# Kernel optimization log

Hardware: AMD Instinct MI355X
Metric: run time of the kernel (lower is better)

The kernel has to match this reference:

```python
import jax, jax.numpy as jnp
import numpy as np

B, T, D = 8, 4096, 768
N_HEADS = 12
HEAD_DIM = D // N_HEADS
N_STATE = 64
ALPHA = 0.1


def setup_inputs() -> dict:
    key = jax.random.key(0)
    k1, k2, k3 = jax.random.split(key, 3)
    H = jax.random.normal(k1, (B, T, D), dtype=jnp.float32)
    prototypes = jax.random.normal(k2, (N_STATE, D), dtype=jnp.float32)
    W_tok = jax.random.normal(k3, (D, D), dtype=jnp.float32) * (1.0 / np.sqrt(D))
    s0 = jnp.zeros((1, N_STATE, D), dtype=jnp.float32)
    return {"H": H, "prototypes": prototypes, "W_tok": W_tok, "s0": s0}


def reference(H, prototypes, W_tok, s0):
    b, t, d = H.shape
    hd = HEAD_DIM
    a = ALPHA
    # q: [B, n_heads, T, head_dim]
    q = (H @ W_tok.T).reshape(b, t, N_HEADS, hd).transpose(0, 2, 1, 3)
    # k: [n_heads, n_state, head_dim]
    k = prototypes.reshape(N_STATE, N_HEADS, hd).transpose(1, 0, 2)
    # score: [B, n_heads, T, n_state]; routing_temp == 1.0
    score = jnp.einsum('bhtd,hmd->bhtm', q, k) / (hd ** 0.5)
    w = jax.nn.softmax(score, axis=-1)
    g = 1.0 - a * w
    # suffix-inclusive product over T: prod_{t'>=t} g[t']
    suffix_inc = jnp.flip(jnp.cumprod(jnp.flip(g, axis=2), axis=2), axis=2)
    suffix_exc = jnp.concatenate(
        [suffix_inc[:, :, 1:, :], jnp.ones_like(suffix_inc[:, :, :1, :])], axis=2)
    w_eff = a * w * suffix_exc  # [B, H, T, n_state]
    h_ph = H.reshape(b, t, N_HEADS, hd).transpose(0, 2, 1, 3)  # [B,H,T,hd]
    s0h = jnp.broadcast_to(s0, (b, N_STATE, d)).reshape(
        b, N_STATE, N_HEADS, hd).transpose(0, 2, 1, 3)  # [B,H,n_state,hd]
    residual = suffix_inc[:, :, 0, :][..., None]  # [B,H,n_state,1]
    s = s0h * residual + jnp.einsum('bhtm,bhtd->bhmd', w_eff, h_ph)
    return s.transpose(0, 2, 1, 3).reshape(b, N_STATE, d)
```

## Files before the change

kernel.cpp:

```cpp
#include <hip/hip_runtime.h>

#define B_ 8
#define T_ 4096
#define D_ 768
#define NH_ 12
#define M_ 64
#define ALPHA_ 0.1f

#define CCH 16
#define CHUNK_T 256

using half8 = __attribute__((ext_vector_type(8))) _Float16;
using short8 = __attribute__((ext_vector_type(8))) short;
using f32x4 = __attribute__((ext_vector_type(4))) float;

__device__ __forceinline__ unsigned int f2h2(float a, float b) {
    unsigned short ua = __builtin_bit_cast(unsigned short, (_Float16)a);
    unsigned short ub = __builtin_bit_cast(unsigned short, (_Float16)b);
    return (unsigned int)ua | ((unsigned int)ub << 16);
}
__device__ __forceinline__ float h2f(unsigned short u) {
    return (float)__builtin_bit_cast(_Float16, u);
}
__device__ __forceinline__ void gload_lds16(const void* g, void* l) {
    __builtin_amdgcn_global_load_lds(
        (const __attribute__((address_space(1))) unsigned int*)g,
        (__attribute__((address_space(3))) unsigned int*)l, 16, 0, 0);
}

__global__ __launch_bounds__(256) void kH16(const float* __restrict__ H,
                                            unsigned short* __restrict__ H16) {
    const int i = blockIdx.x * 256 + threadIdx.x;
#pragma unroll
    for (int j = 0; j < 4; ++j) {
        const int idx = i + j * 1572864;
        const float4 v = reinterpret_cast<const float4*>(H)[idx];
        uint2 pk = {f2h2(v.x, v.y), f2h2(v.z, v.w)};
        reinterpret_cast<uint2*>(H16)[idx] = pk;
    }
}

__global__ __launch_bounds__(256) void kP(const float* __restrict__ proto,
                                          const float* __restrict__ W,
                                          unsigned short* __restrict__ P16) {
    const int et = blockIdx.x;
    const int h  = blockIdx.y;
    const int tid = threadIdx.x;

    __shared__ __align__(16) float Ws[64 * 128];
    __shared__ __align__(16) float Ks[64 * 64];

#pragma unroll
    for (int j = 0; j < 8; ++j) {
        int f = tid + j * 256;
        int i = f >> 5, c4 = f & 31;
        const float4 v = *reinterpret_cast<const float4*>(
            W + (size_t)(h * 64 + i) * D_ + et * 128 + c4 * 4);
        *reinterpret_cast<float4*>(&Ws[i * 128 + c4 * 4]) = v;
    }
#pragma unroll
    for (int j = 0; j < 4; ++j) {
        int f = tid + j * 256;
        int m = f >> 4, i4 = f & 15;
        const float4 v = *reinterpret_cast<const float4*>(
            proto + (size_t)m * D_ + h * 64 + i4 * 4);
        Ks[(i4 * 4 + 0) * 64 + m] = v.x;
        Ks[(i4 * 4 + 1) * 64 + m] = v.y;
        Ks[(i4 * 4 + 2) * 64 + m] = v.z;
        Ks[(i4 * 4 + 3) * 64 + m] = v.w;
    }
    __syncthreads();

    const int m0 = (tid >> 5) * 8;
    const int e0 = (tid & 31) * 4;
    float acc[8][4];
#pragma unroll
    for (int i = 0; i < 8; ++i)
#pragma unroll
        for (int j = 0; j < 4; ++j) acc[i][j] = 0.f;

    for (int i = 0; i < 64; ++i) {
        const float4 bb = *reinterpret_cast<const float4*>(&Ws[i * 128 + e0]);
        const float4 a0 = *reinterpret_cast<const float4*>(&Ks[i * 64 + m0]);
        const float4 a1 = *reinterpret_cast<const float4*>(&Ks[i * 64 + m0 + 4]);
        const float a[8] = {a0.x, a0.y, a0.z, a0.w, a1.x, a1.y, a1.z, a1.w};
#pragma unroll
        for (int mi = 0; mi < 8; ++mi) {
            acc[mi][0] = fmaf(a[mi], bb.x, acc[mi][0]);
            acc[mi][1] = fmaf(a[mi], bb.y, acc[mi][1]);
            acc[mi][2] = fmaf(a[mi], bb.z, acc[mi][2]);
            acc[mi][3] = fmaf(a[mi], bb.w, acc[mi][3]);
        }
    }
#pragma unroll
    for (int mi = 0; mi < 8; ++mi) {
        size_t idx = (size_t)(h * 64 + m0 + mi) * D_ + et * 128 + e0;
        uint2 pk = {f2h2(acc[mi][0] * 0.125f, acc[mi][1] * 0.125f),
                    f2h2(acc[mi][2] * 0.125f, acc[mi][3] * 0.125f)};
        *reinterpret_cast<uint2*>(P16 + idx) = pk;
    }
}

#define LDS_BYTES 69632

__global__ __launch_bounds__(512, 4) void k1(const unsigned short* __restrict__ H16,
                                             const unsigned short* __restrict__ P16,
                                             float* __restrict__ chunkprod,
                                             float* __restrict__ partial) {
    const int p = blockIdx.x;
    const int b = p & 7;
    const int s = p >> 3;
    const int hp = s % 6;
    const int c  = s / 6;
    const int tid = threadIdx.x;
    const int wv  = tid >> 6;
    const int lane = tid & 63;
    const int l15 = lane & 15;
    const int q4  = lane >> 4;
    const int hl  = wv >> 2;
    const int tq  = wv & 3;

    extern __shared__ __align__(16) unsigned char smem[];
    unsigned short* wT = (unsigned short*)(smem);
    unsigned short* Hh = (unsigned short*)(smem + 33792);
    float* segprod = (float*)(smem + 67584);

    const size_t Hrow = (size_t)(b * T_ + c * CHUNK_T);
    const unsigned short* gA = H16 + Hrow * D_;
    const unsigned short* gB = P16 + (size_t)(hp * 2) * 64 * D_;

    f32x4 acc[4][4] = {};

    for (int kt = 0; kt < 12; ++kt) {
        __syncthreads();
#pragma unroll
        for (int j = 0; j < 4; ++j) {
            int sl = j * 512 + tid;
            int r = sl >> 3, gp = sl & 7, g = gp ^ (r & 7);
            gload_lds16(gA + (size_t)r * D_ + kt * 64 + g * 8, smem + sl * 16);
        }
#pragma unroll
        for (int j = 0; j < 2; ++j) {
            int sl = j * 512 + tid;
            int r = (sl & 511) >> 3, gp = sl & 7, g = gp ^ (r & 7);
            gload_lds16(gB + (size_t)(j * 64 + r) * D_ + kt * 64 + g * 8,
                        smem + 32768 + sl * 16);
        }
        __syncthreads();
#pragma unroll
        for (int ks = 0; ks < 2; ++ks) {
            const int gp = ((ks * 4 + q4) ^ (l15 & 7)) * 16;
            half8 af[4], bf[4];
#pragma unroll
            for (int tt = 0; tt < 4; ++tt)
                af[tt] = *reinterpret_cast<const half8*>(
                    smem + (tq * 64 + tt * 16 + l15) * 128 + gp);
#pragma unroll
            for (int mt = 0; mt < 4; ++mt)
                bf[mt] = *reinterpret_cast<const half8*>(
                    smem + 32768 + hl * 8192 + (mt * 16 + l15) * 128 + gp);
#pragma unroll
            for (int tt = 0; tt < 4; ++tt)
#pragma unroll
                for (int mt = 0; mt < 4; ++mt)
                    acc[tt][mt] = __builtin_amdgcn_mfma_f32_16x16x32_f16(
                        af[tt], bf[mt], acc[tt][mt], 0, 0, 0);
        }
    }

#pragma unroll
    for (int tt = 0; tt < 4; ++tt)
#pragma unroll
        for (int rg = 0; rg < 4; ++rg) {
            float e0 = __expf(acc[tt][0][rg]);
            float e1 = __expf(acc[tt][1][rg]);
            float e2 = __expf(acc[tt][2][rg]);
            float e3 = __expf(acc[tt][3][rg]);
            float sm = (e0 + e1) + (e2 + e3);
#pragma unroll
            for (int msk = 1; msk <= 8; msk <<= 1)
                sm += __shfl_xor(sm, msk, 64);
            float inv = __builtin_amdgcn_rcpf(sm);
            acc[tt][0][rg] = e0 * inv;
            acc[tt][1][rg] = e1 * inv;
            acc[tt][2][rg] = e2 * inv;
            acc[tt][3][rg] = e3 * inv;
        }
    __syncthreads();

    const int m_s = tid & 63;
    const int g8  = tid >> 6;

    for (int head = 0; head < 2; ++head) {
        const int h = hp * 2 + head;
        const int chunkIdx = (b * NH_ + h) * CCH + c;
        if (head) __syncthreads();

        if (hl == head) {
#pragma unroll
            for (int tt = 0; tt < 4; ++tt)
#pragma unroll
                for (int mt = 0; mt < 4; ++mt) {
                    uint2 pk = {f2h2(acc[tt][mt][0], acc[tt][mt][1]),
                                f2h2(acc[tt][mt][2], acc[tt][mt][3])};
                    *reinterpret_cast<uint2*>(
                        wT + (mt * 16 + l15) * 264 + tq * 64 + tt * 16 + q4 * 4) = pk;
                }
        }
        {
            const int dp = tid & 31, tg = tid >> 5;
            const unsigned short* src = H16 + (Hrow + tg * 16) * D_ + h * 64 + 2 * dp;
            unsigned short* dst0 = Hh + (2 * dp) * 264 + tg * 16;
            unsigned short* dst1 = Hh + (2 * dp + 1) * 264 + tg * 16;
#pragma unroll
            for (int i = 0; i < 8; ++i) {
                unsigned int a = *reinterpret_cast<const unsigned int*>(
                    src + (size_t)(2 * i) * D_);
                unsigned int bb = *reinterpret_cast<const unsigned int*>(
                    src + (size_t)(2 * i + 1) * D_);
                *reinterpret_cast<unsigned int*>(dst0 + 2 * i) =
                    (a & 0xffffu) | (bb << 16);
                *reinterpret_cast<unsigned int*>(dst1 + 2 * i) =
                    (a >> 16) | (bb & 0xffff0000u);
            }
        }
        __syncthreads();

        {
            unsigned short* rowp = wT + m_s * 264 + g8 * 32;
            float pband = 1.0f;
#pragma unroll
            for (int oct = 0; oct < 4; ++oct) {
                short8 v = *reinterpret_cast<const short8*>(rowp + oct * 8);
#pragma unroll
                for (int j = 0; j < 8; ++j)
                    pband *= fmaf(-ALPHA_, h2f((unsigned short)v[j]), 1.0f);
            }
            segprod[g8 * 64 + m_s] = pband;
            __syncthreads();
            float R = 1.0f;
#pragma unroll
            for (int gg = 1; gg < 8; ++gg)
                if (g8 + gg < 8) R *= segprod[(g8 + gg) * 64 + m_s];
            if (g8 == 0)
                chunkprod[(size_t)chunkIdx * 64 + m_s] = R * pband;
#pragma unroll
            for (int oct = 3; oct >= 0; --oct) {
                short8 v = *reinterpret_cast<const short8*>(rowp + oct * 8);
                short8 o;
#pragma unroll
                for (int j = 7; j >= 0; --j) {
                    float w = h2f((unsigned short)v[j]);
                    _Float16 we = (_Float16)(ALPHA_ * w * R);
                    o[j] = (short)__builtin_bit_cast(unsigned short, we);
                    R *= fmaf(-ALPHA_, w, 1.0f);
                }
                *reinterpret_cast<short8*>(rowp + oct * 8) = o;
            }
        }
        __syncthreads();

        {
            const int mt = wv & 3;
            const int dh = wv >> 2;
            f32x4 pacc[2] = {};
#pragma unroll
            for (int ks = 0; ks < 8; ++ks) {
                half8 a = *reinterpret_cast<const half8*>(
                    wT + (mt * 16 + l15) * 264 + ks * 32 + q4 * 8);
#pragma unroll
                for (int dt = 0; dt < 2; ++dt) {
                    half8 bb = *reinterpret_cast<const half8*>(
                        Hh + (dh * 32 + dt * 16 + l15) * 264 + ks * 32 + q4 * 8);
                    pacc[dt] = __builtin_amdgcn_mfma_f32_16x16x32_f16(
                        a, bb, pacc[dt], 0, 0, 0);
                }
            }
#pragma unroll
            for (int dt = 0; dt < 2; ++dt)
#pragma unroll
                for (int rg = 0; rg < 4; ++rg)
                    partial[((size_t)chunkIdx * 64 + mt * 16 + q4 * 4 + rg) * 64
                            + dh * 32 + dt * 16 + l15] = pacc[dt][rg];
        }
    }
}

__global__ __launch_bounds__(256) void k2(const float* __restrict__ chunkprod,
                                          const float* __restrict__ partial,
                                          const float* __restrict__ s0,
                                          float* __restrict__ out) {
    const int h = blockIdx.x;
    const int b = blockIdx.y;
    const int mg = blockIdx.z;
    const int tid = threadIdx.x;
    const int m  = mg * 16 + (tid >> 4);
    const int d0 = (tid & 15) * 4;

    const size_t cpBase = (size_t)(b * NH_ + h) * CCH;
    float sfx[CCH];
    float run = 1.0f;
#pragma unroll
    for (int c = CCH - 1; c >= 0; --c) {
        sfx[c] = run;
        run *= chunkprod[(cpBase + c) * M_ + m];
    }
    const float4 v0 = *reinterpret_cast<const float4*>(
        s0 + (size_t)m * D_ + h * 64 + d0);
    float4 acc = make_float4(v0.x * run, v0.y * run, v0.z * run, v0.w * run);
#pragma unroll
    for (int c = 0; c < CCH; ++c) {
        const float sv = sfx[c];
        const float4 pp = *reinterpret_cast<const float4*>(
            partial + ((cpBase + c) * M_ + m) * 64 + d0);
        acc.x = fmaf(sv, pp.x, acc.x);
        acc.y = fmaf(sv, pp.y, acc.y);
        acc.z = fmaf(sv, pp.z, acc.z);
        acc.w = fmaf(sv, pp.w, acc.w);
    }
    *reinterpret_cast<float4*>(out + (size_t)(b * M_ + m) * D_ + h * 64 + d0) = acc;
}

extern "C" void kernel_launch(void* const* d_in, const int* in_sizes, int n_in,
                              void* d_out, int out_size, void* d_ws, size_t ws_size,
                              hipStream_t stream) {
    const float* H     = (const float*)d_in[0];
    const float* proto = (const float*)d_in[1];
    const float* W     = (const float*)d_in[2];
    const float* s0    = (const float*)d_in[3];
    float* out = (float*)d_out;

    unsigned short* H16 = (unsigned short*)d_ws;
    unsigned short* P16 = (unsigned short*)((unsigned char*)d_ws + 50331648);
    float* chunkprod = (float*)((unsigned char*)d_ws + 51511296);
    float* partial   = (float*)((unsigned char*)d_ws + 51904512);

    kH16<<<dim3(6144), 256, 0, stream>>>(H, H16);
    kP<<<dim3(6, NH_), 256, 0, stream>>>(proto, W, P16);
    k1<<<dim3(768), 512, LDS_BYTES, stream>>>(H16, P16, chunkprod, partial);
    k2<<<dim3(NH_, B_, 4), 256, 0, stream>>>(chunkprod, partial, s0, out);
}
```

Measured before the change: 226.7 us.

## Double-buffer k1 score GEMM with 32x32 MFMA and prefetch head slices

The score GEMM in k1 now stages 32-wide K slices into two alternating LDS buffers, so global-to-LDS copies for the next step overlap MFMA work on the current one, with one barrier per iteration instead of two. It also switches from 16x16x32 to 32x32x16 f16 MFMA tiles and adapts the softmax reduction and the transposed write-out to the new accumulator layout. The H slices for both heads are loaded into registers early, overlapping them with the softmax and head-0 work. Most block barriers are replaced by an LDS-only wait plus s_barrier, so pending global loads are not drained at each barrier. This raises register pressure, and the ordering of the loads relies on the new barriers being correct.

```diff
diff --git a/kernel.cpp b/kernel.cpp
--- a/kernel.cpp
+++ b/kernel.cpp
@@ -13,6 +13,7 @@
 using half8 = __attribute__((ext_vector_type(8))) _Float16;
 using short8 = __attribute__((ext_vector_type(8))) short;
 using f32x4 = __attribute__((ext_vector_type(4))) float;
+using f32x16 = __attribute__((ext_vector_type(16))) float;
 
 __device__ __forceinline__ unsigned int f2h2(float a, float b) {
     unsigned short ua = __builtin_bit_cast(unsigned short, (_Float16)a);
@@ -26,6 +27,10 @@
     __builtin_amdgcn_global_load_lds(
         (const __attribute__((address_space(1))) unsigned int*)g,
         (__attribute__((address_space(3))) unsigned int*)l, 16, 0, 0);
+}
+__device__ __forceinline__ void barrier_lgkm() {
+    asm volatile("s_waitcnt lgkmcnt(0)" ::: "memory");
+    __builtin_amdgcn_s_barrier();
 }
 
 __global__ __launch_bounds__(256) void kH16(const float* __restrict__ H,
@@ -102,6 +107,22 @@
 }
 
 #define LDS_BYTES 69632
+
+#define STAGE(KT, BUF) do {                                                    \
+    _Pragma("unroll")                                                          \
+    for (int j_ = 0; j_ < 2; ++j_) {                                           \
+        int sl_ = j_ * 512 + tid;                                              \
+        int r_ = sl_ >> 2, gp_ = sl_ & 3, g_ = gp_ ^ ((r_ >> 1) & 3);          \
+        gload_lds16(gA + (size_t)r_ * D_ + (KT) * 32 + g_ * 8,                 \
+                    smem + (BUF) * 16384 + sl_ * 16);                          \
+    }                                                                          \
+    {                                                                          \
+        int sl_ = tid;                                                         \
+        int r_ = sl_ >> 2, gp_ = sl_ & 3, g_ = gp_ ^ ((r_ >> 1) & 3);          \
+        gload_lds16(gB + (size_t)r_ * D_ + (KT) * 32 + g_ * 8,                 \
+                    smem + 32768 + (BUF) * 8192 + sl_ * 16);                   \
+    }                                                                          \
+} while (0)
 
 __global__ __launch_bounds__(512, 4) void k1(const unsigned short* __restrict__ H16,
                                              const unsigned short* __restrict__ P16,
@@ -117,6 +138,8 @@
     const int lane = tid & 63;
     const int l15 = lane & 15;
     const int q4  = lane >> 4;
+    const int l31 = lane & 31;
+    const int q1  = lane >> 5;
     const int hl  = wv >> 2;
     const int tq  = wv & 3;
 
@@ -129,64 +152,63 @@
     const unsigned short* gA = H16 + Hrow * D_;
     const unsigned short* gB = P16 + (size_t)(hp * 2) * 64 * D_;
 
-    f32x4 acc[4][4] = {};
-
-    for (int kt = 0; kt < 12; ++kt) {
+    f32x16 acc2[2][2] = {};
+
+    const int sx = (l31 >> 1) & 3;
+    STAGE(0, 0);
+    for (int kt = 0; kt < 24; ++kt) {
         __syncthreads();
-#pragma unroll
-        for (int j = 0; j < 4; ++j) {
-            int sl = j * 512 + tid;
-            int r = sl >> 3, gp = sl & 7, g = gp ^ (r & 7);
-            gload_lds16(gA + (size_t)r * D_ + kt * 64 + g * 8, smem + sl * 16);
-        }
-#pragma unroll
-        for (int j = 0; j < 2; ++j) {
-            int sl = j * 512 + tid;
-            int r = (sl & 511) >> 3, gp = sl & 7, g = gp ^ (r & 7);
-            gload_lds16(gB + (size_t)(j * 64 + r) * D_ + kt * 64 + g * 8,
-                        smem + 32768 + sl * 16);
-        }
-        __syncthreads();
-#pragma unroll
-        for (int ks = 0; ks < 2; ++ks) {
-            const int gp = ((ks * 4 + q4) ^ (l15 & 7)) * 16;
-            half8 af[4], bf[4];
-#pragma unroll
-            for (int tt = 0; tt < 4; ++tt)
-                af[tt] = *reinterpret_cast<const half8*>(
-                    smem + (tq * 64 + tt * 16 + l15) * 128 + gp);
-#pragma unroll
-            for (int mt = 0; mt < 4; ++mt)
-                bf[mt] = *reinterpret_cast<const half8*>(
-                    smem + 32768 + hl * 8192 + (mt * 16 + l15) * 128 + gp);
-#pragma unroll
-            for (int tt = 0; tt < 4; ++tt)
-#pragma unroll
-                for (int mt = 0; mt < 4; ++mt)
-                    acc[tt][mt] = __builtin_amdgcn_mfma_f32_16x16x32_f16(
-                        af[tt], bf[mt], acc[tt][mt], 0, 0, 0);
-        }
-    }
-
-#pragma unroll
-    for (int tt = 0; tt < 4; ++tt)
-#pragma unroll
-        for (int rg = 0; rg < 4; ++rg) {
-            float e0 = __expf(acc[tt][0][rg]);
-            float e1 = __expf(acc[tt][1][rg]);
-            float e2 = __expf(acc[tt][2][rg]);
-            float e3 = __expf(acc[tt][3][rg]);
-            float sm = (e0 + e1) + (e2 + e3);
-#pragma unroll
-            for (int msk = 1; msk <= 8; msk <<= 1)
+        if (kt < 23) STAGE(kt + 1, (kt + 1) & 1);
+        const int cur = kt & 1;
+        const unsigned char* Ab = smem + cur * 16384 + (tq * 64 + l31) * 64;
+        const unsigned char* Bb = smem + 32768 + cur * 8192 + (hl * 64 + l31) * 64;
+        half8 af[2][2], bf[2][2];
+#pragma unroll
+        for (int tt2 = 0; tt2 < 2; ++tt2)
+#pragma unroll
+            for (int ks = 0; ks < 2; ++ks)
+                af[tt2][ks] = *reinterpret_cast<const half8*>(
+                    Ab + tt2 * 2048 + (((ks * 2 + q1) ^ sx) * 16));
+#pragma unroll
+        for (int mt2 = 0; mt2 < 2; ++mt2)
+#pragma unroll
+            for (int ks = 0; ks < 2; ++ks)
+                bf[mt2][ks] = *reinterpret_cast<const half8*>(
+                    Bb + mt2 * 2048 + (((ks * 2 + q1) ^ sx) * 16));
+#pragma unroll
+        for (int ks = 0; ks < 2; ++ks)
+#pragma unroll
+            for (int tt2 = 0; tt2 < 2; ++tt2)
+#pragma unroll
+                for (int mt2 = 0; mt2 < 2; ++mt2)
+                    acc2[tt2][mt2] = __builtin_amdgcn_mfma_f32_32x32x16_f16(
+                        af[tt2][ks], bf[mt2][ks], acc2[tt2][mt2], 0, 0, 0);
+    }
+
+    const int dp = tid & 31, tg5 = tid >> 5;
+    const unsigned short* hsrc = H16 + (Hrow + tg5 * 16) * D_ + (hp * 2) * 64 + 2 * dp;
+    unsigned int av[8], bw[8];
+#pragma unroll
+    for (int i = 0; i < 8; ++i) {
+        av[i] = *reinterpret_cast<const unsigned int*>(hsrc + (size_t)(2 * i) * D_);
+        bw[i] = *reinterpret_cast<const unsigned int*>(hsrc + (size_t)(2 * i + 1) * D_);
+    }
+
+#pragma unroll
+    for (int tt2 = 0; tt2 < 2; ++tt2)
+#pragma unroll
+        for (int rg = 0; rg < 16; ++rg) {
+            float e0 = __expf(acc2[tt2][0][rg]);
+            float e1 = __expf(acc2[tt2][1][rg]);
+            float sm = e0 + e1;
+#pragma unroll
+            for (int msk = 1; msk <= 16; msk <<= 1)
                 sm += __shfl_xor(sm, msk, 64);
             float inv = __builtin_amdgcn_rcpf(sm);
-            acc[tt][0][rg] = e0 * inv;
-            acc[tt][1][rg] = e1 * inv;
-            acc[tt][2][rg] = e2 * inv;
-            acc[tt][3][rg] = e3 * inv;
-        }
-    __syncthreads();
+            acc2[tt2][0][rg] = e0 * inv;
+            acc2[tt2][1][rg] = e1 * inv;
+        }
+    barrier_lgkm();
 
     const int m_s = tid & 63;
     const int g8  = tid >> 6;
@@ -194,37 +216,43 @@
     for (int head = 0; head < 2; ++head) {
         const int h = hp * 2 + head;
         const int chunkIdx = (b * NH_ + h) * CCH + c;
-        if (head) __syncthreads();
 
         if (hl == head) {
 #pragma unroll
-            for (int tt = 0; tt < 4; ++tt)
-#pragma unroll
-                for (int mt = 0; mt < 4; ++mt) {
-                    uint2 pk = {f2h2(acc[tt][mt][0], acc[tt][mt][1]),
-                                f2h2(acc[tt][mt][2], acc[tt][mt][3])};
-                    *reinterpret_cast<uint2*>(
-                        wT + (mt * 16 + l15) * 264 + tq * 64 + tt * 16 + q4 * 4) = pk;
-                }
+            for (int tt2 = 0; tt2 < 2; ++tt2)
+#pragma unroll
+                for (int mt2 = 0; mt2 < 2; ++mt2)
+#pragma unroll
+                    for (int rb = 0; rb < 4; ++rb) {
+                        int t = tq * 64 + tt2 * 32 + rb * 8 + q1 * 4;
+                        uint2 pk = {f2h2(acc2[tt2][mt2][rb * 4 + 0],
+                                         acc2[tt2][mt2][rb * 4 + 1]),
+                                    f2h2(acc2[tt2][mt2][rb * 4 + 2],
+                                         acc2[tt2][mt2][rb * 4 + 3])};
+                        *reinterpret_cast<uint2*>(
+                            wT + (mt2 * 32 + l31) * 264 + t) = pk;
+                    }
         }
         {
-            const int dp = tid & 31, tg = tid >> 5;
-            const unsigned short* src = H16 + (Hrow + tg * 16) * D_ + h * 64 + 2 * dp;
-            unsigned short* dst0 = Hh + (2 * dp) * 264 + tg * 16;
-            unsigned short* dst1 = Hh + (2 * dp + 1) * 264 + tg * 16;
+            unsigned short* dst0 = Hh + (2 * dp) * 264 + tg5 * 16;
+            unsigned short* dst1 = Hh + (2 * dp + 1) * 264 + tg5 * 16;
 #pragma unroll
             for (int i = 0; i < 8; ++i) {
-                unsigned int a = *reinterpret_cast<const unsigned int*>(
-                    src + (size_t)(2 * i) * D_);
-                unsigned int bb = *reinterpret_cast<const unsigned int*>(
-                    src + (size_t)(2 * i + 1) * D_);
                 *reinterpret_cast<unsigned int*>(dst0 + 2 * i) =
-                    (a & 0xffffu) | (bb << 16);
+                    (av[i] & 0xffffu) | (bw[i] << 16);
                 *reinterpret_cast<unsigned int*>(dst1 + 2 * i) =
-                    (a >> 16) | (bb & 0xffff0000u);
-            }
-        }
-        __syncthreads();
+                    (av[i] >> 16) | (bw[i] & 0xffff0000u);
+            }
+        }
+        if (head == 0) {
+            const unsigned short* hs1 = hsrc + 64;
+#pragma unroll
+            for (int i = 0; i < 8; ++i) {
+                av[i] = *reinterpret_cast<const unsigned int*>(hs1 + (size_t)(2 * i) * D_);
+                bw[i] = *reinterpret_cast<const unsigned int*>(hs1 + (size_t)(2 * i + 1) * D_);
+            }
+        }
+        barrier_lgkm();
 
         {
             unsigned short* rowp = wT + m_s * 264 + g8 * 32;
@@ -237,7 +265,7 @@
                     pband *= fmaf(-ALPHA_, h2f((unsigned short)v[j]), 1.0f);
             }
             segprod[g8 * 64 + m_s] = pband;
-            __syncthreads();
+            barrier_lgkm();
             float R = 1.0f;
 #pragma unroll
             for (int gg = 1; gg < 8; ++gg)
@@ -258,7 +286,7 @@
                 *reinterpret_cast<short8*>(rowp + oct * 8) = o;
             }
         }
-        __syncthreads();
+        barrier_lgkm();
 
         {
             const int mt = wv & 3;
@@ -283,6 +311,7 @@
                     partial[((size_t)chunkIdx * 64 + mt * 16 + q4 * 4 + rg) * 64
                             + dh * 32 + dt * 16 + l15] = pacc[dt][rg];
         }
+        if (head == 0) barrier_lgkm();
     }
 }
 
```

Measured after the change: 238.3 us. 5.1% more time.

## Double-buffer k1 score GEMM K-loop with 32-wide K steps

Applied to the files above, without the earlier changes.

The score GEMM in k1 now uses two LDS buffers with a K step of 32 instead of a single buffer with a K step of 64. The next tile's global-to-LDS loads are issued before the MFMAs on the current tile, so one barrier per iteration replaces two. The aim is to overlap global load latency with MFMA work. The trade-off is twice as many K iterations and a 4-way XOR swizzle instead of 8-way, which may add bank conflicts. The per-head barrier is also moved from the start of the second head to the end of the first, which is equivalent.

```diff
diff --git a/kernel.cpp b/kernel.cpp
--- a/kernel.cpp
+++ b/kernel.cpp
@@ -102,6 +102,22 @@
 }
 
 #define LDS_BYTES 69632
+
+#define STAGE(KT, BUF) do {                                                    \
+    _Pragma("unroll")                                                          \
+    for (int j_ = 0; j_ < 2; ++j_) {                                           \
+        int sl_ = j_ * 512 + tid;                                              \
+        int r_ = sl_ >> 2, gp_ = sl_ & 3, g_ = gp_ ^ (r_ & 3);                 \
+        gload_lds16(gA + (size_t)r_ * D_ + (KT) * 32 + g_ * 8,                 \
+                    smem + (BUF) * 16384 + sl_ * 16);                          \
+    }                                                                          \
+    {                                                                          \
+        int sl_ = tid;                                                         \
+        int r_ = sl_ >> 2, gp_ = sl_ & 3, g_ = gp_ ^ (r_ & 3);                 \
+        gload_lds16(gB + (size_t)r_ * D_ + (KT) * 32 + g_ * 8,                 \
+                    smem + 32768 + (BUF) * 8192 + sl_ * 16);                   \
+    }                                                                          \
+} while (0)
 
 __global__ __launch_bounds__(512, 4) void k1(const unsigned short* __restrict__ H16,
                                              const unsigned short* __restrict__ P16,
@@ -131,41 +147,28 @@
 
     f32x4 acc[4][4] = {};
 
-    for (int kt = 0; kt < 12; ++kt) {
+    const int gp = (q4 ^ (l15 & 3)) * 16;
+    STAGE(0, 0);
+    for (int kt = 0; kt < 24; ++kt) {
         __syncthreads();
-#pragma unroll
-        for (int j = 0; j < 4; ++j) {
-            int sl = j * 512 + tid;
-            int r = sl >> 3, gp = sl & 7, g = gp ^ (r & 7);
-            gload_lds16(gA + (size_t)r * D_ + kt * 64 + g * 8, smem + sl * 16);
-        }
-#pragma unroll
-        for (int j = 0; j < 2; ++j) {
-            int sl = j * 512 + tid;
-            int r = (sl & 511) >> 3, gp = sl & 7, g = gp ^ (r & 7);
-            gload_lds16(gB + (size_t)(j * 64 + r) * D_ + kt * 64 + g * 8,
-                        smem + 32768 + sl * 16);
-        }
-        __syncthreads();
-#pragma unroll
-        for (int ks = 0; ks < 2; ++ks) {
-            const int gp = ((ks * 4 + q4) ^ (l15 & 7)) * 16;
-            half8 af[4], bf[4];
-#pragma unroll
-            for (int tt = 0; tt < 4; ++tt)
-                af[tt] = *reinterpret_cast<const half8*>(
-                    smem + (tq * 64 + tt * 16 + l15) * 128 + gp);
+        if (kt < 23) STAGE(kt + 1, (kt + 1) & 1);
+        const unsigned char* Ab = smem + (kt & 1) * 16384;
+        const unsigned char* Bb = smem + 32768 + (kt & 1) * 8192 + hl * 4096;
+        half8 af[4], bf[4];
+#pragma unroll
+        for (int tt = 0; tt < 4; ++tt)
+            af[tt] = *reinterpret_cast<const half8*>(
+                Ab + (tq * 64 + tt * 16 + l15) * 64 + gp);
+#pragma unroll
+        for (int mt = 0; mt < 4; ++mt)
+            bf[mt] = *reinterpret_cast<const half8*>(
+                Bb + (mt * 16 + l15) * 64 + gp);
+#pragma unroll
+        for (int tt = 0; tt < 4; ++tt)
 #pragma unroll
             for (int mt = 0; mt < 4; ++mt)
-                bf[mt] = *reinterpret_cast<const half8*>(
-                    smem + 32768 + hl * 8192 + (mt * 16 + l15) * 128 + gp);
-#pragma unroll
-            for (int tt = 0; tt < 4; ++tt)
-#pragma unroll
-                for (int mt = 0; mt < 4; ++mt)
-                    acc[tt][mt] = __builtin_amdgcn_mfma_f32_16x16x32_f16(
-                        af[tt], bf[mt], acc[tt][mt], 0, 0, 0);
-        }
+                acc[tt][mt] = __builtin_amdgcn_mfma_f32_16x16x32_f16(
+                    af[tt], bf[mt], acc[tt][mt], 0, 0, 0);
     }
 
 #pragma unroll
@@ -194,7 +197,6 @@
     for (int head = 0; head < 2; ++head) {
         const int h = hp * 2 + head;
         const int chunkIdx = (b * NH_ + h) * CCH + c;
-        if (head) __syncthreads();
 
         if (hl == head) {
 #pragma unroll
@@ -283,6 +285,7 @@
                     partial[((size_t)chunkIdx * 64 + mt * 16 + q4 * 4 + rg) * 64
                             + dh * 32 + dt * 16 + l15] = pacc[dt][rg];
         }
+        if (head == 0) __syncthreads();
     }
 }
 
```

After: 229.6 us. No clear change (+1.3%).

## Fuse fp32-to-fp16 conversion of H into main kernel with register prefetch

Applied to the files above, without the earlier changes.

Removes the separate H-to-fp16 conversion kernel and its 48MB workspace. The main kernel now reads fp32 H directly, converts it to fp16 in registers and stores it to LDS, prefetching the next k-tile into registers while MFMAs run. The per-head H gather also reads fp32 and converts. This avoids writing and re-reading an fp16 copy of H, at the cost of reading twice the bytes per load in k1, extra VGPRs and moving one barrier.

```diff
diff --git a/kernel.cpp b/kernel.cpp
--- a/kernel.cpp
+++ b/kernel.cpp
@@ -26,18 +26,6 @@
     __builtin_amdgcn_global_load_lds(
         (const __attribute__((address_space(1))) unsigned int*)g,
         (__attribute__((address_space(3))) unsigned int*)l, 16, 0, 0);
-}
-
-__global__ __launch_bounds__(256) void kH16(const float* __restrict__ H,
-                                            unsigned short* __restrict__ H16) {
-    const int i = blockIdx.x * 256 + threadIdx.x;
-#pragma unroll
-    for (int j = 0; j < 4; ++j) {
-        const int idx = i + j * 1572864;
-        const float4 v = reinterpret_cast<const float4*>(H)[idx];
-        uint2 pk = {f2h2(v.x, v.y), f2h2(v.z, v.w)};
-        reinterpret_cast<uint2*>(H16)[idx] = pk;
-    }
 }
 
 __global__ __launch_bounds__(256) void kP(const float* __restrict__ proto,
@@ -103,7 +91,28 @@
 
 #define LDS_BYTES 69632
 
-__global__ __launch_bounds__(512, 4) void k1(const unsigned short* __restrict__ H16,
+#define LOADA(KT) do {                                                         \
+    _Pragma("unroll")                                                          \
+    for (int j_ = 0; j_ < 4; ++j_) {                                           \
+        const float* p_ = gAf + (size_t)(ar + j_ * 64) * D_ + (KT) * 64 + ag * 8; \
+        av0[j_] = *reinterpret_cast<const float4*>(p_);                        \
+        av1[j_] = *reinterpret_cast<const float4*>(p_ + 4);                    \
+    }                                                                          \
+} while (0)
+
+#define WRITEA() do {                                                          \
+    _Pragma("unroll")                                                          \
+    for (int j_ = 0; j_ < 4; ++j_) {                                           \
+        uint4 w_;                                                              \
+        w_.x = f2h2(av0[j_].x, av0[j_].y);                                     \
+        w_.y = f2h2(av0[j_].z, av0[j_].w);                                     \
+        w_.z = f2h2(av1[j_].x, av1[j_].y);                                     \
+        w_.w = f2h2(av1[j_].z, av1[j_].w);                                     \
+        *reinterpret_cast<uint4*>(smem + (j_ * 512 + tid) * 16) = w_;          \
+    }                                                                          \
+} while (0)
+
+__global__ __launch_bounds__(512, 4) void k1(const float* __restrict__ Hf,
                                              const unsigned short* __restrict__ P16,
                                              float* __restrict__ chunkprod,
                                              float* __restrict__ partial) {
@@ -126,19 +135,18 @@
     float* segprod = (float*)(smem + 67584);
 
     const size_t Hrow = (size_t)(b * T_ + c * CHUNK_T);
-    const unsigned short* gA = H16 + Hrow * D_;
+    const float* gAf = Hf + Hrow * D_;
     const unsigned short* gB = P16 + (size_t)(hp * 2) * 64 * D_;
 
     f32x4 acc[4][4] = {};
 
+    const int ar = tid >> 3;
+    const int ag = (tid & 7) ^ (ar & 7);
+    float4 av0[4], av1[4];
+
+    LOADA(0);
     for (int kt = 0; kt < 12; ++kt) {
         __syncthreads();
-#pragma unroll
-        for (int j = 0; j < 4; ++j) {
-            int sl = j * 512 + tid;
-            int r = sl >> 3, gp = sl & 7, g = gp ^ (r & 7);
-            gload_lds16(gA + (size_t)r * D_ + kt * 64 + g * 8, smem + sl * 16);
-        }
 #pragma unroll
         for (int j = 0; j < 2; ++j) {
             int sl = j * 512 + tid;
@@ -146,7 +154,9 @@
             gload_lds16(gB + (size_t)(j * 64 + r) * D_ + kt * 64 + g * 8,
                         smem + 32768 + sl * 16);
         }
+        WRITEA();
         __syncthreads();
+        if (kt < 11) LOADA(kt + 1);
 #pragma unroll
         for (int ks = 0; ks < 2; ++ks) {
             const int gp = ((ks * 4 + q4) ^ (l15 & 7)) * 16;
@@ -194,7 +204,6 @@
     for (int head = 0; head < 2; ++head) {
         const int h = hp * 2 + head;
         const int chunkIdx = (b * NH_ + h) * CCH + c;
-        if (head) __syncthreads();
 
         if (hl == head) {
 #pragma unroll
@@ -209,19 +218,17 @@
         }
         {
             const int dp = tid & 31, tg = tid >> 5;
-            const unsigned short* src = H16 + (Hrow + tg * 16) * D_ + h * 64 + 2 * dp;
+            const float* src = Hf + (Hrow + tg * 16) * D_ + h * 64 + 2 * dp;
             unsigned short* dst0 = Hh + (2 * dp) * 264 + tg * 16;
             unsigned short* dst1 = Hh + (2 * dp + 1) * 264 + tg * 16;
 #pragma unroll
             for (int i = 0; i < 8; ++i) {
-                unsigned int a = *reinterpret_cast<const unsigned int*>(
+                const float2 a = *reinterpret_cast<const float2*>(
                     src + (size_t)(2 * i) * D_);
-                unsigned int bb = *reinterpret_cast<const unsigned int*>(
+                const float2 bb = *reinterpret_cast<const float2*>(
                     src + (size_t)(2 * i + 1) * D_);
-                *reinterpret_cast<unsigned int*>(dst0 + 2 * i) =
-                    (a & 0xffffu) | (bb << 16);
-                *reinterpret_cast<unsigned int*>(dst1 + 2 * i) =
-                    (a >> 16) | (bb & 0xffff0000u);
+                *reinterpret_cast<unsigned int*>(dst0 + 2 * i) = f2h2(a.x, bb.x);
+                *reinterpret_cast<unsigned int*>(dst1 + 2 * i) = f2h2(a.y, bb.y);
             }
         }
         __syncthreads();
@@ -283,6 +290,7 @@
                     partial[((size_t)chunkIdx * 64 + mt * 16 + q4 * 4 + rg) * 64
                             + dh * 32 + dt * 16 + l15] = pacc[dt][rg];
         }
+        if (head == 0) __syncthreads();
     }
 }
 
@@ -330,13 +338,11 @@
     const float* s0    = (const float*)d_in[3];
     float* out = (float*)d_out;
 
-    unsigned short* H16 = (unsigned short*)d_ws;
-    unsigned short* P16 = (unsigned short*)((unsigned char*)d_ws + 50331648);
-    float* chunkprod = (float*)((unsigned char*)d_ws + 51511296);
-    float* partial   = (float*)((unsigned char*)d_ws + 51904512);
-
-    kH16<<<dim3(6144), 256, 0, stream>>>(H, H16);
+    unsigned short* P16 = (unsigned short*)d_ws;
+    float* chunkprod = (float*)((unsigned char*)d_ws + 1179648);
+    float* partial   = (float*)((unsigned char*)d_ws + 1572864);
+
     kP<<<dim3(6, NH_), 256, 0, stream>>>(proto, W, P16);
-    k1<<<dim3(768), 512, LDS_BYTES, stream>>>(H16, P16, chunkprod, partial);
+    k1<<<dim3(768), 512, LDS_BYTES, stream>>>(H, P16, chunkprod, partial);
     k2<<<dim3(NH_, B_, 4), 256, 0, stream>>>(chunkprod, partial, s0, out);
 }
```

New measurement: 229.7 us. About the same (+1.3%).
